# Kernel optimization log

Measured on AMD Instinct MI355X. Metric: run time of the kernel, lower is better.

## Reference

```python
import jax, jax.numpy as jnp
import numpy as np
import math
from jax import lax

NUM_POS = 128        # random_choice in pos_neg_sampling
NUM_TOT = 256        # pos + (128 + negative_padding) always totals 256
POS_W = 10.0         # positive_weight in compute_loss


def _conv(x, w, b, pad):
    y = lax.conv_general_dilated(x, w, (1, 1), pad,
                                 dimension_numbers=('NCHW', 'OIHW', 'NCHW'))
    return y + b[None, :, None, None]


def make_anchor_box(img_h, img_w, gh, gw):
    # torch.range(0, W, W/(gw-1)) == inclusive linspace with gw points
    xs = jnp.linspace(0.0, float(img_w), gw)
    ys = jnp.linspace(0.0, float(img_h), gh)
    gx, gy = jnp.meshgrid(xs, ys, indexing='ij')          # (gw, gh) like torch.meshgrid
    xy = jnp.stack([gx.reshape(-1), gy.reshape(-1)], -1).reshape(gh, gw, 2)
    whs = []
    for area in (128 * 128, 256 * 256, 512 * 512):
        for wr, hr in ((1, 1), (2, 1), (1, 2)):
            u = math.sqrt(area / (wr * hr))
            whs.append((wr * u, hr * u))
    wh = jnp.asarray(whs, jnp.float32)                    # (9, 2)
    xy9 = jnp.broadcast_to(xy[:, :, None, :], (gh, gw, 9, 2))
    wh9 = jnp.broadcast_to(wh[None, None], (gh, gw, 9, 2))
    boxes = jnp.concatenate([xy9, xy9 + wh9], -1)         # x1,y1,x2,y2
    return boxes.reshape(-1, 4)


def pairwise_iou(t, a):
    # t: [T,4], a: [A,4], xyxy -> [T,A]
    lt = jnp.maximum(t[:, None, :2], a[None, :, :2])
    rb = jnp.minimum(t[:, None, 2:], a[None, :, 2:])
    wh = jnp.clip(rb - lt, 0.0)
    inter = wh[..., 0] * wh[..., 1]
    at = (t[:, 2] - t[:, 0]) * (t[:, 3] - t[:, 1])
    aa = (a[:, 2] - a[:, 0]) * (a[:, 3] - a[:, 1])
    return inter / (at[:, None] + aa[None, :] - inter)


def box_encode(anchor, bbox):
    awh = anchor[:, 2:] - anchor[:, :2]
    bwh = bbox[:, 2:] - bbox[:, :2]
    ac = anchor[:, :2] + awh / 2
    bc = bbox[:, :2] + bwh / 2
    dxy = (bc - ac) / awh
    dwh = jnp.log(bwh / awh)
    return jnp.concatenate([dxy, dwh], 1)


def rpn_forward(x, target, conv_w, conv_b, bbox_w, bbox_b, score_w, score_b,
                img_h, img_w):
    gh, gw = x.shape[-2], x.shape[-1]
    h = jax.nn.relu(_conv(x[None], conv_w, conv_b, 'SAME'))
    bbox = jax.nn.relu(_conv(h, bbox_w, bbox_b, 'VALID')).reshape(-1, 4)   # [A,4]
    score = jax.nn.relu(_conv(h, score_w, score_b, 'VALID')).reshape(-1, 2)  # [A,2]
    anchors = make_anchor_box(img_h, img_w, gh, gw)                        # [A,4]

    iou = pairwise_iou(target, anchors)                                    # [T,A]
    max_iou = iou.max(0)
    tgt_idx = jnp.argmax(iou, 0)

    # deterministic replacement for np.random.choice sampling (fixed shapes)
    pos_score = jnp.where(max_iou > 0.7, max_iou, -1.0)
    pos_vals, pos_idx = lax.top_k(pos_score, NUM_POS)
    pos_valid = pos_vals > 0.0
    n_pos = jnp.sum(pos_valid.astype(jnp.int32))

    neg_score = jnp.where(max_iou < 0.3, 1.0 - max_iou, -1.0)
    neg_vals, neg_idx = lax.top_k(neg_score, NUM_TOT)
    neg_valid = (neg_vals > 0.0) & (jnp.arange(NUM_TOT) < (NUM_TOT - n_pos))

    bbox_pred = bbox[pos_idx]                                              # [128,4]
    scores_sel = score[jnp.concatenate([pos_idx, neg_idx])]                # [384,2]
    valid = jnp.concatenate([pos_valid, neg_valid]).astype(jnp.float32)

    tgt_scores = jnp.concatenate([
        jnp.tile(jnp.asarray([[1.0, 0.0]], jnp.float32), (NUM_POS, 1)),
        jnp.tile(jnp.asarray([[0.0, 1.0]], jnp.float32), (NUM_TOT, 1))], 0)

    matched = target[tgt_idx[pos_idx]]
    treg = box_encode(anchors[pos_idx], matched)

    ce = -jnp.sum(tgt_scores * jax.nn.log_softmax(scores_sel, -1), -1)
    score_loss = jnp.sum(ce * valid) / jnp.maximum(jnp.sum(valid), 1.0)

    d = bbox_pred - treg
    sl1 = jnp.where(jnp.abs(d) < 1.0, 0.5 * d * d, jnp.abs(d) - 0.5)
    pm = pos_valid.astype(jnp.float32)[:, None]
    reg_loss = jnp.sum(sl1 * pm) / jnp.maximum(jnp.sum(pm) * 4.0, 1.0)

    return score_loss + POS_W * reg_loss


def setup_inputs():
    key = jax.random.key(0)
    ks = jax.random.split(key, 8)
    cin, gh, gw, nt = 512, 128, 128, 64
    x = jax.random.normal(ks[0], (cin, gh, gw), jnp.float32)
    cxy = jax.random.uniform(ks[1], (nt, 2), minval=300.0, maxval=1748.0)
    wh = jax.random.uniform(ks[2], (nt, 2), minval=64.0, maxval=512.0)
    target = jnp.concatenate([cxy - wh / 2, cxy + wh / 2], -1)
    conv_w = jax.random.normal(ks[3], (cin, cin, 3, 3), jnp.float32) * 0.02
    conv_b = jnp.zeros((cin,), jnp.float32)
    bbox_w = jax.random.normal(ks[4], (36, cin, 1, 1), jnp.float32) * 0.02
    bbox_b = jnp.zeros((36,), jnp.float32)
    score_w = jax.random.normal(ks[5], (18, cin, 1, 1), jnp.float32) * 0.02
    score_b = jnp.zeros((18,), jnp.float32)
    return {'x': x, 'target': target, 'conv_w': conv_w, 'conv_b': conv_b,
            'bbox_w': bbox_w, 'bbox_b': bbox_b, 'score_w': score_w,
            'score_b': score_b, 'img_h': 2048, 'img_w': 2048}


def reference(x, target, conv_w, conv_b, bbox_w, bbox_b, score_w, score_b,
              img_h, img_w):
    return rpn_forward(x, target, conv_w, conv_b, bbox_w, bbox_b,
                       score_w, score_b, img_h, img_w)
```

## Files before the change

kernel.cpp:

```cpp
#include <hip/hip_runtime.h>
#include <cstdint>
#include <cstddef>

typedef unsigned long long ull;
typedef __bf16 bf16x8 __attribute__((ext_vector_type(8)));
typedef float f32x4 __attribute__((ext_vector_type(4)));

#define NA     147456
#define NT     64
#define KDIM   4608
#define NTASK  1280
#define CAND_CAP 4096
#define KSPLIT 4
#define NIOUB  576
#define NPREPB 1152
#define NIMCB  2880

#define OFF_WB2   0
#define OFF_P2    4718592
#define OFF_H4    16515072
#define OFF_MIOU  27000832
#define OFF_CAND  27590656
#define OFF_CPB   28770304
#define OFF_CBZ   28772608
#define OFF_NPOS  28774912
#define OFF_TREG  28774920
#define OFF_TASKS 28776968
#define OFF_OUT   28782088

#define UANC 90.509667991878f
__device__ __constant__ float WKa[9] = {128.0f, 2.0f*UANC, UANC, 256.0f, 4.0f*UANC, 2.0f*UANC, 512.0f, 8.0f*UANC, 4.0f*UANC};
__device__ __constant__ float HKa[9] = {128.0f, UANC, 2.0f*UANC, 256.0f, 2.0f*UANC, 4.0f*UANC, 512.0f, 4.0f*UANC, 8.0f*UANC};

__device__ __forceinline__ float iou_one(float x1, float y1, float x2, float y2, float4 t) {
#pragma clang fp contract(off)
  float ltx = fmaxf(t.x, x1), lty = fmaxf(t.y, y1);
  float rbx = fminf(t.z, x2), rby = fminf(t.w, y2);
  float wx = fmaxf(rbx - ltx, 0.0f);
  float wy = fmaxf(rby - lty, 0.0f);
  float inter = wx * wy;
  float at = (t.z - t.x) * (t.w - t.y);
  float aa = (x2 - x1) * (y2 - y1);
  return inter / ((at + aa) - inter);
}

__device__ __forceinline__ unsigned short f2bf(float f) {
  unsigned int u = __float_as_uint(f);
  unsigned int r = (u + 0x7fffu + ((u >> 16) & 1u)) >> 16;
  return (unsigned short)r;
}

__global__ __launch_bounds__(256) void k_pi(const float* __restrict__ cw,
    unsigned short* __restrict__ Wb2,
    const float* __restrict__ tgt, const int* __restrict__ imw,
    const int* __restrict__ imh, float* __restrict__ miou,
    ull* __restrict__ cand, int* __restrict__ cpb, int* __restrict__ cbz) {
  int blk = blockIdx.x;
  int tid = threadIdx.x;
  if (blk >= NIOUB) {
    int idx = (blk - NIOUB) * 256 + tid;
    int m = idx & 511, kc = idx >> 9;
    const float4* src = (const float4*)(cw + (size_t)m * KDIM + kc * 8);
    float4 v0 = src[0], v1 = src[1];
    unsigned short o[8] = {f2bf(v0.x), f2bf(v0.y), f2bf(v0.z), f2bf(v0.w),
                           f2bf(v1.x), f2bf(v1.y), f2bf(v1.z), f2bf(v1.w)};
    *(uint4*)(Wb2 + (size_t)idx * 8) = *(const uint4*)o;
    return;
  }
  __shared__ float4 ts[NT];
  __shared__ int wz[4], wc[4];
  if (tid < NT) ts[tid] = ((const float4*)tgt)[tid];
  __syncthreads();
  int a = blk * 256 + tid;
  int k = a % 9;
  int pq = a / 9;
  int p = pq >> 7, q = pq & 127;
  float dx = (float)(*imw) / 127.0f;
  float dyl = (float)(*imh) / 127.0f;
  float x1 = (float)p * dx, y1 = (float)q * dyl;
  float x2 = x1 + WKa[k], y2 = y1 + HKa[k];
  float best = -1.0f;
  #pragma unroll 8
  for (int t = 0; t < NT; ++t) best = fmaxf(best, iou_one(x1, y1, x2, y2, ts[t]));
  miou[a] = best;
  int lane = tid & 63, w = tid >> 6;
  ull bz = __ballot(best == 0.0f);
  bool isc = best > 0.7f;
  ull bc = __ballot(isc);
  if (lane == 0) { wz[w] = (int)__popcll(bz); wc[w] = (int)__popcll(bc); }
  __syncthreads();
  if (tid == 0) {
    cbz[blk] = wz[0] + wz[1] + wz[2] + wz[3];
    cpb[blk] = wc[0] + wc[1] + wc[2] + wc[3];
  }
  if (isc) {
    int woff = 0;
    for (int i = 0; i < w; ++i) woff += wc[i];
    int rank = woff + (int)__popcll(bc & ((1ull << lane) - 1ull));
    cand[blk * 256 + rank] = ((ull)__float_as_uint(best) << 32) | (ull)(0xFFFFFFFFu - (unsigned)a);
  }
}

__global__ __launch_bounds__(256) void k_sel(const float* __restrict__ miou,
    const ull* __restrict__ cand, const int* __restrict__ cpb,
    const int* __restrict__ cbz, const float* __restrict__ tgt,
    const int* __restrict__ imw, const int* __restrict__ imh,
    int* __restrict__ nposp, float* __restrict__ treg, int* __restrict__ tasks) {
  __shared__ ull keys[CAND_CAP];
  __shared__ int cpbL[576];
  __shared__ int base576[577];
  __shared__ int nzbase[145];
  __shared__ float4 ts[NT];
  __shared__ int posi[128];
  __shared__ int negA[256];
  __shared__ int wtot[4];
  __shared__ int wsum[4];
  int tid = threadIdx.x;
  int lane = tid & 63;
  if (tid < NT) ts[tid] = ((const float4*)tgt)[tid];
  for (int i = tid; i < 576; i += 256) cpbL[i] = cpb[i];
  __syncthreads();
  int e0 = 0, e1 = 0, sA = 0, scanA = 0;
  if (tid < 192) {
    e0 = cpbL[3 * tid]; e1 = cpbL[3 * tid + 1]; int e2 = cpbL[3 * tid + 2];
    sA = e0 + e1 + e2;
    scanA = sA;
    for (int off = 1; off < 64; off <<= 1) {
      int v = __shfl_up(scanA, off);
      if (lane >= off) scanA += v;
    }
    if (lane == 63) wtot[tid >> 6] = scanA;
  }
  int sB = 0, scanB = 0;
  if (tid < 144) {
    int4 cz4 = *(const int4*)(cbz + 4 * tid);
    sB = cz4.x + cz4.y + cz4.z + cz4.w;
    scanB = sB;
    for (int off = 1; off < 64; off <<= 1) {
      int v = __shfl_up(scanB, off);
      if (lane >= off) scanB += v;
    }
    bool last = (tid < 128) ? (lane == 63) : (tid == 143);
    if (last) wsum[tid >> 6] = scanB;
  }
  __syncthreads();
  if (tid < 192) {
    int w = tid >> 6;
    int woff = 0;
    for (int i = 0; i < w; ++i) woff += wtot[i];
    int excl = woff + scanA - sA;
    base576[3 * tid]     = excl;
    base576[3 * tid + 1] = excl + e0;
    base576[3 * tid + 2] = excl + e0 + e1;
    if (tid == 191) base576[576] = excl + sA;
  }
  if (tid < 144) {
    int w = tid >> 6;
    int woff = 0;
    for (int i = 0; i < w; ++i) woff += wsum[i];
    nzbase[tid] = woff + scanB - sB;
    if (tid == 143) nzbase[144] = woff + scanB;
  }
  __syncthreads();
  int cnt = base576[NIOUB]; if (cnt > CAND_CAP) cnt = CAND_CAP;
  for (int i = tid; i < CAND_CAP; i += 256) if (i >= cnt) keys[i] = 0ull;
  for (int j = tid; j < NIOUB; j += 256) {
    int b = base576[j], c = base576[j + 1] - b;
    for (int e = 0; e < c; ++e) {
      int dst = b + e;
      if (dst < CAND_CAP) keys[dst] = cand[j * 256 + e];
    }
  }
  __syncthreads();
  int np;
  if (cnt <= 128) {
    np = cnt;
  } else {
    int n = 256; while (n < cnt) n <<= 1;
    for (int size = 2; size <= n; size <<= 1)
      for (int stride = size >> 1; stride > 0; stride >>= 1) {
        __syncthreads();
        for (int t = tid; t < n / 2; t += 256) {
          int i = 2 * t - (t & (stride - 1));
          int j = i + stride;
          ull a = keys[i], b = keys[j];
          bool desc = ((i & size) == 0);
          if (desc ? (a < b) : (a > b)) { keys[i] = b; keys[j] = a; }
        }
      }
    np = 128;
  }
  __syncthreads();
  if (tid < np) posi[tid] = (int)(0xFFFFFFFFu - (unsigned)(keys[tid] & 0xFFFFFFFFull));
  if (tid == 0) *nposp = np;
  __syncthreads();
  int w = tid >> 6;
  for (int j = 0; j < 144; ++j) {
    if (nzbase[j] >= 256) break;
    int a0 = j * 1024 + tid * 4;
    float4 m4 = *(const float4*)(miou + a0);
    int f0 = (m4.x == 0.0f), f1 = (m4.y == 0.0f), f2 = (m4.z == 0.0f), f3 = (m4.w == 0.0f);
    int tsum = f0 + f1 + f2 + f3;
    int scan = tsum;
    for (int off = 1; off < 64; off <<= 1) {
      int v = __shfl_up(scan, off);
      if (lane >= off) scan += v;
    }
    if (lane == 63) wsum[w] = scan;
    __syncthreads();
    int woff = nzbase[j];
    for (int i = 0; i < w; ++i) woff += wsum[i];
    int r = woff + scan - tsum;
    if (f0) { if (r < 256) negA[r] = a0;     r++; }
    if (f1) { if (r < 256) negA[r] = a0 + 1; r++; }
    if (f2) { if (r < 256) negA[r] = a0 + 2; r++; }
    if (f3) { if (r < 256) negA[r] = a0 + 3;      }
    __syncthreads();
  }
  __syncthreads();
  if (tid < np) {
    int a = posi[tid];
    int k = a % 9; int pq = a / 9; int p = pq >> 7, q = pq & 127;
    float dx = (float)(*imw) / 127.0f, dyl = (float)(*imh) / 127.0f;
    float x1 = (float)p * dx, y1 = (float)q * dyl;
    float x2 = x1 + WKa[k], y2 = y1 + HKa[k];
    float best = -1.0f; int bt = 0;
    for (int t = 0; t < NT; ++t) {
      float v = iou_one(x1, y1, x2, y2, ts[t]);
      if (v > best) { best = v; bt = t; }
    }
    float4 m = ts[bt];
    float aw = x2 - x1, ah = y2 - y1;
    float acx = x1 + aw * 0.5f, acy = y1 + ah * 0.5f;
    float bwd = m.z - m.x, bhd = m.w - m.y;
    float bcx = m.x + bwd * 0.5f, bcy = m.y + bhd * 0.5f;
    treg[tid * 4 + 0] = (bcx - acx) / aw;
    treg[tid * 4 + 1] = (bcy - acy) / ah;
    treg[tid * 4 + 2] = logf(bwd / aw);
    treg[tid * 4 + 3] = logf(bhd / ah);
  }
  for (int t = tid; t < NTASK; t += 256) {
    int rec = 0;
    if (t < 768) {
      int s = t / 6, jj = t - s * 6;
      if (s < np) {
        int a = posi[s];
        int f, wr, xx;
        if (jj < 4) { f = 4 * a; wr = f >> 14; xx = (f & 127) + jj; }
        else        { f = 2 * a; wr = 36 + (f >> 14); xx = (f & 127) + (jj - 4); }
        int yy = (f >> 7) & 127;
        rec = (int)(0x80000000u | ((unsigned)wr << 16) | ((unsigned)yy << 8) | (unsigned)xx);
      }
    } else {
      int s = (t - 768) >> 1, jj = (t - 768) & 1;
      if (s < 256 - np) {
        int a = negA[s];
        int f = 2 * a; int wr = 36 + (f >> 14); int yy = (f >> 7) & 127; int xx = (f & 127) + jj;
        rec = (int)(0x80000000u | ((unsigned)wr << 16) | ((unsigned)yy << 8) | (unsigned)xx);
      }
    }
    tasks[t] = rec;
  }
}

__global__ __launch_bounds__(256) void k_im2col(const float* __restrict__ x,
    const int* __restrict__ tasks, unsigned short* __restrict__ P2) {
  int idx = blockIdx.x * 256 + threadIdx.x;
  int t = idx % NTASK;
  int kc = idx / NTASK;
  int rec = tasks[t];
  unsigned short o[8];
  if (rec < 0) {
    int py = (rec >> 8) & 127, px = rec & 127;
    #pragma unroll
    for (int j = 0; j < 8; ++j) {
      int k = kc * 8 + j;
      int cin = k / 9;
      int rr = k - cin * 9;
      int dy = rr / 3;
      int yy = py + dy - 1, xx = px + (rr - dy * 3) - 1;
      float v = (yy >= 0 && yy < 128 && xx >= 0 && xx < 128)
                  ? x[cin * 16384 + yy * 128 + xx] : 0.0f;
      o[j] = f2bf(v);
    }
  } else {
    #pragma unroll
    for (int j = 0; j < 8; ++j) o[j] = 0;
  }
  *(uint4*)(P2 + (size_t)idx * 8) = *(const uint4*)o;
}

__global__ __launch_bounds__(256) void k_mfma(const unsigned short* __restrict__ Wb2,
    const unsigned short* __restrict__ P2, const int* __restrict__ nposp,
    float* __restrict__ H4) {
  int npos = *nposp;
  int tt0 = blockIdx.x * 128;
  int posend = 6 * npos, negend = 768 + 2 * (256 - npos);
  if (!((tt0 < posend) || ((tt0 + 128 > 768) && (tt0 < negend)))) return;
  int c0 = blockIdx.y * 128;
  int ks = blockIdx.z;
  int tid = threadIdx.x;
  int wave = tid >> 6, lane = tid & 63;
  int quad = lane >> 4, r = lane & 15;
  int m_base = c0 + (wave & 1) * 64;
  int n_base = tt0 + (wave >> 1) * 64;
  int kc0 = ks * 144 + quad;
  const bf16x8* Ab = (const bf16x8*)Wb2 + ((size_t)kc0 * 512 + m_base + r);
  const bf16x8* Bb = (const bf16x8*)P2 + ((size_t)kc0 * NTASK + n_base + r);

  f32x4 acc[4][4];
  #pragma unroll
  for (int i = 0; i < 4; ++i)
    #pragma unroll
    for (int j = 0; j < 4; ++j) acc[i][j] = (f32x4){0.f, 0.f, 0.f, 0.f};

  bf16x8 a[4], b[4];
  #pragma unroll
  for (int mi = 0; mi < 4; ++mi) a[mi] = Ab[mi * 16];
  #pragma unroll
  for (int ni = 0; ni < 4; ++ni) b[ni] = Bb[ni * 16];

  for (int s = 0; s < 36; ++s) {
    bf16x8 an[4], bn[4];
    if (s < 35) {
      const bf16x8* An = Ab + (size_t)(s + 1) * 4 * 512;
      const bf16x8* Bn = Bb + (size_t)(s + 1) * 4 * NTASK;
      #pragma unroll
      for (int mi = 0; mi < 4; ++mi) an[mi] = An[mi * 16];
      #pragma unroll
      for (int ni = 0; ni < 4; ++ni) bn[ni] = Bn[ni * 16];
    }
    #pragma unroll
    for (int mi = 0; mi < 4; ++mi)
      #pragma unroll
      for (int ni = 0; ni < 4; ++ni)
        acc[mi][ni] = __builtin_amdgcn_mfma_f32_16x16x32_bf16(a[mi], b[ni], acc[mi][ni], 0, 0, 0);
    if (s < 35) {
      #pragma unroll
      for (int mi = 0; mi < 4; ++mi) a[mi] = an[mi];
      #pragma unroll
      for (int ni = 0; ni < 4; ++ni) b[ni] = bn[ni];
    }
  }
  size_t hb = (size_t)ks * NTASK;
  #pragma unroll
  for (int mi = 0; mi < 4; ++mi) {
    int c = m_base + mi * 16 + quad * 4;
    #pragma unroll
    for (int ni = 0; ni < 4; ++ni) {
      int t = n_base + ni * 16 + r;
      *(f32x4*)(H4 + (hb + t) * 512 + c) = acc[mi][ni];
    }
  }
}

__global__ __launch_bounds__(256) void k_out(const float* __restrict__ H4,
    const int* __restrict__ tasks,
    const float* __restrict__ cb, const float* __restrict__ bw,
    const float* __restrict__ bb, const float* __restrict__ sw,
    const float* __restrict__ sb, float* __restrict__ outv) {
  int wave = threadIdx.x >> 6, lane = threadIdx.x & 63;
  int t = blockIdx.x * 4 + wave;
  int rec = tasks[t];
  if (rec >= 0) return;
  int wr = (rec >> 16) & 63;
  const float* wrow = (wr < 36) ? (bw + wr * 512) : (sw + (wr - 36) * 512);
  float s = 0.0f;
  #pragma unroll
  for (int it = 0; it < 8; ++it) {
    int c = it * 64 + lane;
    size_t o = (size_t)t * 512 + c;
    float hv = H4[o] + H4[o + 1280 * 512] + H4[o + 2 * 1280 * 512] + H4[o + 3 * 1280 * 512] + cb[c];
    s = fmaf(fmaxf(hv, 0.0f), wrow[c], s);
  }
  #pragma unroll
  for (int off = 32; off > 0; off >>= 1) s += __shfl_down(s, off);
  if (lane == 0) {
    float b = (wr < 36) ? bb[wr] : sb[wr - 36];
    outv[t] = fmaxf(s + b, 0.0f);
  }
}

__global__ __launch_bounds__(256) void k_loss(const float* __restrict__ outv,
    const float* __restrict__ treg, const int* __restrict__ nposp,
    float* __restrict__ out) {
  __shared__ float r1[256], r2[256];
  int tid = threadIdx.x;
  int np = *nposp;
  float ce = 0.0f;
  for (int r = tid; r < 384; r += 256) {
    bool valid = (r < 128) ? (r < np) : ((r - 128) < 256 - np);
    if (valid) {
      int t0 = (r < 128) ? (r * 6 + 4) : (768 + 2 * (r - 128));
      float s0 = outv[t0], s1 = outv[t0 + 1];
      float mm = fmaxf(s0, s1);
      float lse = mm + logf(expf(s0 - mm) + expf(s1 - mm));
      ce += lse - ((r < 128) ? s0 : s1);
    }
  }
  float rg = 0.0f;
  for (int r = tid; r < 512; r += 256) {
    if ((r >> 2) < np) {
      float d = outv[(r >> 2) * 6 + (r & 3)] - treg[r];
      float ad = fabsf(d);
      rg += (ad < 1.0f) ? 0.5f * d * d : ad - 0.5f;
    }
  }
  r1[tid] = ce; r2[tid] = rg;
  __syncthreads();
  for (int s = 128; s > 0; s >>= 1) {
    if (tid < s) { r1[tid] += r1[tid + s]; r2[tid] += r2[tid + s]; }
    __syncthreads();
  }
  if (tid == 0) {
    float score_loss = r1[0] / 256.0f;
    float reg_loss = r2[0] / fmaxf(4.0f * (float)np, 1.0f);
    out[0] = score_loss + 10.0f * reg_loss;
  }
}

extern "C" void kernel_launch(void* const* d_in, const int* in_sizes, int n_in,
                              void* d_out, int out_size, void* d_ws, size_t ws_size,
                              hipStream_t stream) {
  const float* x   = (const float*)d_in[0];
  const float* tgt = (const float*)d_in[1];
  const float* cw  = (const float*)d_in[2];
  const float* cb  = (const float*)d_in[3];
  const float* bw  = (const float*)d_in[4];
  const float* bb  = (const float*)d_in[5];
  const float* sw  = (const float*)d_in[6];
  const float* sb  = (const float*)d_in[7];
  const int* imh   = (const int*)d_in[8];
  const int* imw   = (const int*)d_in[9];

  char* ws = (char*)d_ws;
  unsigned short* Wb2 = (unsigned short*)(ws + OFF_WB2);
  unsigned short* P2  = (unsigned short*)(ws + OFF_P2);
  float* H4    = (float*)(ws + OFF_H4);
  float* miou  = (float*)(ws + OFF_MIOU);
  ull*   cand  = (ull*)(ws + OFF_CAND);
  int*   cpb   = (int*)(ws + OFF_CPB);
  int*   cbz   = (int*)(ws + OFF_CBZ);
  int*   nposp = (int*)(ws + OFF_NPOS);
  float* treg  = (float*)(ws + OFF_TREG);
  int*   tasks = (int*)(ws + OFF_TASKS);
  float* outv  = (float*)(ws + OFF_OUT);
  float* out   = (float*)d_out;

  k_pi    <<<dim3(NIOUB + NPREPB), dim3(256), 0, stream>>>(cw, Wb2, tgt, imw, imh, miou, cand, cpb, cbz);
  k_sel   <<<dim3(1),              dim3(256), 0, stream>>>(miou, cand, cpb, cbz, tgt, imw, imh, nposp, treg, tasks);
  k_im2col<<<dim3(NIMCB),          dim3(256), 0, stream>>>(x, tasks, P2);
  k_mfma  <<<dim3(10, 4, KSPLIT),  dim3(256), 0, stream>>>(Wb2, P2, nposp, H4);
  k_out   <<<dim3(320),            dim3(256), 0, stream>>>(H4, tasks, cb, bw, bb, sw, sb, outv);
  k_loss  <<<dim3(1),              dim3(256), 0, stream>>>(outv, treg, nposp, out);
}
```

Measured before the change: 183.2 us.

## Transpose input to pixel-major and reorder GEMM K as tap-major for coalesced im2col

Reorders the GEMM K dimension from (cin, tap) to (tap, cin) in both the weight conversion and im2col, and adds a transpose of x into a pixel-major channel-last buffer. The transpose runs as extra blocks inside the single-block selection kernel so the two overlap. im2col then reads 8 contiguous channels with two float4 loads per thread instead of 8 scattered loads with per-element bounds checks. The cost is a full 32 MB transpose of x and a larger workspace, and the weight conversion now does strided reads.

```diff
diff --git a/kernel.cpp b/kernel.cpp
--- a/kernel.cpp
+++ b/kernel.cpp
@@ -14,19 +14,21 @@
 #define KSPLIT 4
 #define NIOUB  576
 #define NPREPB 1152
+#define NTRB   2048
 #define NIMCB  2880
 
 #define OFF_WB2   0
 #define OFF_P2    4718592
 #define OFF_H4    16515072
-#define OFF_MIOU  27000832
-#define OFF_CAND  27590656
-#define OFF_CPB   28770304
-#define OFF_CBZ   28772608
-#define OFF_NPOS  28774912
-#define OFF_TREG  28774920
-#define OFF_TASKS 28776968
-#define OFF_OUT   28782088
+#define OFF_XT    27000832
+#define OFF_MIOU  60555264
+#define OFF_CAND  61145088
+#define OFF_CPB   62324736
+#define OFF_CBZ   62327040
+#define OFF_NPOS  62329344
+#define OFF_TREG  62329352
+#define OFF_TASKS 62331400
+#define OFF_OUT   62336520
 
 #define UANC 90.509667991878f
 __device__ __constant__ float WKa[9] = {128.0f, 2.0f*UANC, UANC, 256.0f, 4.0f*UANC, 2.0f*UANC, 512.0f, 8.0f*UANC, 4.0f*UANC};
@@ -60,11 +62,12 @@
   if (blk >= NIOUB) {
     int idx = (blk - NIOUB) * 256 + tid;
     int m = idx & 511, kc = idx >> 9;
-    const float4* src = (const float4*)(cw + (size_t)m * KDIM + kc * 8);
-    float4 v0 = src[0], v1 = src[1];
-    unsigned short o[8] = {f2bf(v0.x), f2bf(v0.y), f2bf(v0.z), f2bf(v0.w),
-                           f2bf(v1.x), f2bf(v1.y), f2bf(v1.z), f2bf(v1.w)};
-    *(uint4*)(Wb2 + (size_t)idx * 8) = *(const uint4*)o;
+    int r = kc >> 6, c8 = kc & 63;
+    const float* src = cw + (size_t)m * KDIM + (size_t)(c8 * 8) * 9 + r;
+    unsigned short o[8];
+    #pragma unroll
+    for (int j = 0; j < 8; ++j) o[j] = f2bf(src[j * 9]);
+    *(uint4*)(Wb2 + ((size_t)kc * 512 + m) * 8) = *(const uint4*)o;
     return;
   }
   __shared__ float4 ts[NT];
@@ -105,7 +108,8 @@
     const ull* __restrict__ cand, const int* __restrict__ cpb,
     const int* __restrict__ cbz, const float* __restrict__ tgt,
     const int* __restrict__ imw, const int* __restrict__ imh,
-    int* __restrict__ nposp, float* __restrict__ treg, int* __restrict__ tasks) {
+    int* __restrict__ nposp, float* __restrict__ treg, int* __restrict__ tasks,
+    const float* __restrict__ x, float* __restrict__ xt) {
   __shared__ ull keys[CAND_CAP];
   __shared__ int cpbL[576];
   __shared__ int base576[577];
@@ -116,6 +120,31 @@
   __shared__ int wtot[4];
   __shared__ int wsum[4];
   int tid = threadIdx.x;
+  if (blockIdx.x != 0) {
+    float* tile = (float*)keys;
+    int tb = blockIdx.x - 1;
+    int pix0 = (tb & 255) * 64;
+    int cin0 = (tb >> 8) * 64;
+    int pr = tid & 15, cr = tid >> 4;
+    #pragma unroll
+    for (int i = 0; i < 4; ++i) {
+      int cin = cr + i * 16;
+      float4 v = *(const float4*)(x + (size_t)(cin0 + cin) * 16384 + pix0 + pr * 4);
+      tile[cin * 65 + pr * 4 + 0] = v.x;
+      tile[cin * 65 + pr * 4 + 1] = v.y;
+      tile[cin * 65 + pr * 4 + 2] = v.z;
+      tile[cin * 65 + pr * 4 + 3] = v.w;
+    }
+    __syncthreads();
+    #pragma unroll
+    for (int i = 0; i < 4; ++i) {
+      int pix = cr + i * 16;
+      float4 v = {tile[(pr * 4 + 0) * 65 + pix], tile[(pr * 4 + 1) * 65 + pix],
+                  tile[(pr * 4 + 2) * 65 + pix], tile[(pr * 4 + 3) * 65 + pix]};
+      *(float4*)(xt + (size_t)(pix0 + pix) * 512 + cin0 + pr * 4) = v;
+    }
+    return;
+  }
   int lane = tid & 63;
   if (tid < NT) ts[tid] = ((const float4*)tgt)[tid];
   for (int i = tid; i < 576; i += 256) cpbL[i] = cpb[i];
@@ -263,31 +292,32 @@
   }
 }
 
-__global__ __launch_bounds__(256) void k_im2col(const float* __restrict__ x,
+__global__ __launch_bounds__(256) void k_im2col(const float* __restrict__ xt,
     const int* __restrict__ tasks, unsigned short* __restrict__ P2) {
   int idx = blockIdx.x * 256 + threadIdx.x;
-  int t = idx % NTASK;
-  int kc = idx / NTASK;
+  int t = idx / 576;
+  int kc = idx - t * 576;
+  int r = kc >> 6, c8 = kc & 63;
   int rec = tasks[t];
   unsigned short o[8];
+  bool valid = false;
+  int pix = 0;
   if (rec < 0) {
     int py = (rec >> 8) & 127, px = rec & 127;
-    #pragma unroll
-    for (int j = 0; j < 8; ++j) {
-      int k = kc * 8 + j;
-      int cin = k / 9;
-      int rr = k - cin * 9;
-      int dy = rr / 3;
-      int yy = py + dy - 1, xx = px + (rr - dy * 3) - 1;
-      float v = (yy >= 0 && yy < 128 && xx >= 0 && xx < 128)
-                  ? x[cin * 16384 + yy * 128 + xx] : 0.0f;
-      o[j] = f2bf(v);
-    }
+    int dy = r / 3;
+    int yy = py + dy - 1, xx = px + (r - dy * 3) - 1;
+    if (yy >= 0 && yy < 128 && xx >= 0 && xx < 128) { valid = true; pix = yy * 128 + xx; }
+  }
+  if (valid) {
+    const float4* src = (const float4*)(xt + (size_t)pix * 512 + c8 * 8);
+    float4 v0 = src[0], v1 = src[1];
+    o[0] = f2bf(v0.x); o[1] = f2bf(v0.y); o[2] = f2bf(v0.z); o[3] = f2bf(v0.w);
+    o[4] = f2bf(v1.x); o[5] = f2bf(v1.y); o[6] = f2bf(v1.z); o[7] = f2bf(v1.w);
   } else {
     #pragma unroll
     for (int j = 0; j < 8; ++j) o[j] = 0;
   }
-  *(uint4*)(P2 + (size_t)idx * 8) = *(const uint4*)o;
+  *(uint4*)(P2 + ((size_t)kc * NTASK + t) * 8) = *(const uint4*)o;
 }
 
 __global__ __launch_bounds__(256) void k_mfma(const unsigned short* __restrict__ Wb2,
@@ -437,6 +467,7 @@
   unsigned short* Wb2 = (unsigned short*)(ws + OFF_WB2);
   unsigned short* P2  = (unsigned short*)(ws + OFF_P2);
   float* H4    = (float*)(ws + OFF_H4);
+  float* xt    = (float*)(ws + OFF_XT);
   float* miou  = (float*)(ws + OFF_MIOU);
   ull*   cand  = (ull*)(ws + OFF_CAND);
   int*   cpb   = (int*)(ws + OFF_CPB);
@@ -448,8 +479,8 @@
   float* out   = (float*)d_out;
 
   k_pi    <<<dim3(NIOUB + NPREPB), dim3(256), 0, stream>>>(cw, Wb2, tgt, imw, imh, miou, cand, cpb, cbz);
-  k_sel   <<<dim3(1),              dim3(256), 0, stream>>>(miou, cand, cpb, cbz, tgt, imw, imh, nposp, treg, tasks);
-  k_im2col<<<dim3(NIMCB),          dim3(256), 0, stream>>>(x, tasks, P2);
+  k_sel   <<<dim3(1 + NTRB),       dim3(256), 0, stream>>>(miou, cand, cpb, cbz, tgt, imw, imh, nposp, treg, tasks, x, xt);
+  k_im2col<<<dim3(NIMCB),          dim3(256), 0, stream>>>(xt, tasks, P2);
   k_mfma  <<<dim3(10, 4, KSPLIT),  dim3(256), 0, stream>>>(Wb2, P2, nposp, H4);
   k_out   <<<dim3(320),            dim3(256), 0, stream>>>(H4, tasks, cb, bw, bb, sw, sb, outv);
   k_loss  <<<dim3(1),              dim3(256), 0, stream>>>(outv, treg, nposp, out);
```

Measured after the change: 185.8 us. Within noise of the previous version (+1.4%).
